# Performance work log

Measured on AMD Instinct MI355X. Metric: run time of the kernel, lower is better.

The kernel has to match this reference:

```python
import jax, jax.numpy as jnp
import numpy as np

N_DIM = 4096
N_HEAD = 32
N_KVHEAD = 8
HEAD_DIM = N_DIM // N_HEAD  # 128
N_REP = N_HEAD // N_KVHEAD  # 4
BATCH = 1
SEQ = 2048


def _rope(x, cos, sin):
    # x: [b, s, h, d]; cos/sin: [s, d//2]. Pairs (even, odd) rotated as complex mult.
    b, s, h, d = x.shape
    xp = x.reshape(b, s, h, d // 2, 2)
    xe, xo = xp[..., 0], xp[..., 1]
    c = cos[None, :, None, :]
    si = sin[None, :, None, :]
    oe = xe * c - xo * si
    oo = xe * si + xo * c
    return jnp.stack([oe, oo], axis=-1).reshape(b, s, h, d)


def setup_inputs() -> dict:
    key = jax.random.key(0)
    ks = jax.random.split(key, 5)
    x = jax.random.normal(ks[0], (BATCH, SEQ, N_DIM), dtype=jnp.float32)
    # rotary frequencies (standard RoPE table)
    inv_freq = 1.0 / (10000.0 ** (np.arange(0, HEAD_DIM, 2, dtype=np.float32) / HEAD_DIM))
    angles = np.arange(SEQ, dtype=np.float32)[:, None] * inv_freq[None, :]  # [S, d/2]
    freqs_cos = jnp.asarray(np.cos(angles), dtype=jnp.float32)
    freqs_sin = jnp.asarray(np.sin(angles), dtype=jnp.float32)
    std = 0.006
    wq = jax.random.normal(ks[1], (N_HEAD * HEAD_DIM, N_DIM), dtype=jnp.float32) * std
    wk = jax.random.normal(ks[2], (N_KVHEAD * HEAD_DIM, N_DIM), dtype=jnp.float32) * std
    wv = jax.random.normal(ks[3], (N_KVHEAD * HEAD_DIM, N_DIM), dtype=jnp.float32) * std
    wo = jax.random.normal(ks[4], (N_DIM, N_DIM), dtype=jnp.float32) * std
    return {"x": x, "freqs_cos": freqs_cos, "freqs_sin": freqs_sin,
            "wq": wq, "wk": wk, "wv": wv, "wo": wo}


def reference(x, freqs_cos, freqs_sin, wq, wk, wv, wo):
    b, s, _ = x.shape
    d = 2 * freqs_cos.shape[-1]
    h = wq.shape[0] // d
    hk = wk.shape[0] // d
    n_rep = h // hk

    q = (x @ wq.T).reshape(b, s, h, d)
    k = (x @ wk.T).reshape(b, s, hk, d)
    v = (x @ wv.T).reshape(b, s, hk, d)
    q = _rope(q, freqs_cos, freqs_sin)
    k = _rope(k, freqs_cos, freqs_sin)

    # GQA attention without materializing repeat_kv: group q heads per kv head.
    qg = q.reshape(b, s, hk, n_rep, d)
    scale = 1.0 / jnp.sqrt(jnp.float32(d))
    # scores: [b, hk, n_rep, q_pos, k_pos]
    scores = jnp.einsum('bqhrd,bkhd->bhrqk', qg, k) * scale
    causal = jnp.tril(jnp.ones((s, s), dtype=bool))
    scores = jnp.where(causal[None, None, None, :, :], scores, -jnp.inf)
    attn = jax.nn.softmax(scores, axis=-1)
    out = jnp.einsum('bhrqk,bkhd->bqhrd', attn, v).reshape(b, s, h * d)
    return out @ wo.T
```

## Files before the change

kernel.cpp:

```cpp
#include <hip/hip_runtime.h>

using short8 = __attribute__((ext_vector_type(8))) short;
using f32x4  = __attribute__((ext_vector_type(4))) float;

#define SEQ   2048
#define NDIM  4096
#define NH    32
#define NKV   8
#define HD    128
#define ATT_SCALE 0.08838834764831845f

static __device__ __forceinline__ unsigned short f2bf(float f) {
    unsigned int u = __float_as_uint(f);
    u += 0x7fffu + ((u >> 16) & 1u);
    return (unsigned short)(u >> 16);
}

static __device__ __forceinline__ void gload16(const unsigned short* g, unsigned short* l) {
    __builtin_amdgcn_global_load_lds((const __attribute__((address_space(1))) unsigned int*)g,
                                     (__attribute__((address_space(3))) unsigned int*)l,
                                     16, 0, 0);
}

__global__ __launch_bounds__(256) void cvt_kernel(const float* __restrict__ src,
                                                  unsigned short* __restrict__ dst, int n) {
    int i = blockIdx.x * blockDim.x + threadIdx.x;
    if (i * 4 >= n) return;
    float4 v = ((const float4*)src)[i];
    ushort4 o;
    o.x = f2bf(v.x); o.y = f2bf(v.y); o.z = f2bf(v.z); o.w = f2bf(v.w);
    ((ushort4*)dst)[i] = o;
}

__global__ __launch_bounds__(256) void gemm_bt(const unsigned short* __restrict__ A,
                                               const unsigned short* __restrict__ B,
                                               float* __restrict__ C, int M, int N, int K) {
    __shared__ unsigned short Alds[128 * 32];
    __shared__ unsigned short Blds[128 * 32];
    int tid  = threadIdx.x;
    int wid  = tid >> 6, lane = tid & 63;
    int wr   = wid >> 1, wc  = wid & 1;
    int l15  = lane & 15, hg = lane >> 4;
    long mbase = (long)blockIdx.y * 128;
    long nbase = (long)blockIdx.x * 128;

    f32x4 acc[4][4];
#pragma unroll
    for (int i = 0; i < 4; i++)
#pragma unroll
        for (int j = 0; j < 4; j++) acc[i][j] = f32x4{0.f, 0.f, 0.f, 0.f};

    int c0 = wid * 2, c1 = wid * 2 + 1;
    int srow0 = c0 * 16 + (lane >> 2);
    int srow1 = c1 * 16 + (lane >> 2);
    int scol  = (lane & 3) * 8;
    const unsigned short* Ap0 = A + (mbase + srow0) * (long)K + scol;
    const unsigned short* Ap1 = A + (mbase + srow1) * (long)K + scol;
    const unsigned short* Bp0 = B + (nbase + srow0) * (long)K + scol;
    const unsigned short* Bp1 = B + (nbase + srow1) * (long)K + scol;

    for (int k0 = 0; k0 < K; k0 += 32) {
        __syncthreads();
        gload16(Ap0 + k0, &Alds[c0 * 512]);
        gload16(Ap1 + k0, &Alds[c1 * 512]);
        gload16(Bp0 + k0, &Blds[c0 * 512]);
        gload16(Bp1 + k0, &Blds[c1 * 512]);
        __syncthreads();

        short8 af[4], bf[4];
#pragma unroll
        for (int mi = 0; mi < 4; mi++)
            af[mi] = *(const short8*)&Alds[(wr * 64 + mi * 16 + l15) * 32 + hg * 8];
#pragma unroll
        for (int ni = 0; ni < 4; ni++)
            bf[ni] = *(const short8*)&Blds[(wc * 64 + ni * 16 + l15) * 32 + hg * 8];
#pragma unroll
        for (int mi = 0; mi < 4; mi++)
#pragma unroll
            for (int ni = 0; ni < 4; ni++)
                acc[mi][ni] = __builtin_amdgcn_mfma_f32_16x16x32_bf16(af[mi], bf[ni], acc[mi][ni], 0, 0, 0);
    }

#pragma unroll
    for (int mi = 0; mi < 4; mi++) {
        long row = mbase + wr * 64 + mi * 16 + hg * 4;
#pragma unroll
        for (int ni = 0; ni < 4; ni++) {
            long col = nbase + wc * 64 + ni * 16 + l15;
            float* cp = C + row * N + col;
#pragma unroll
            for (int r = 0; r < 4; r++) cp[(long)r * N] = acc[mi][ni][r];
        }
    }
}

__global__ __launch_bounds__(256) void rope_kernel(const float* __restrict__ X,
                                                   const float* __restrict__ cosb,
                                                   const float* __restrict__ sinb,
                                                   unsigned short* __restrict__ out,
                                                   int hmask, int sshift, int rowstride, float scale) {
    int i = blockIdx.x * blockDim.x + threadIdx.x;
    int p = i & 63;
    int h = (i >> 6) & hmask;
    int s = i >> sshift;
    long off = (long)s * rowstride + h * 128 + 2 * p;
    float2 q = *(const float2*)(X + off);
    float c  = cosb[s * 64 + p];
    float si = sinb[s * 64 + p];
    float oe = (q.x * c - q.y * si) * scale;
    float oo = (q.x * si + q.y * c) * scale;
    ushort2 o;
    o.x = f2bf(oe); o.y = f2bf(oo);
    *(ushort2*)(out + off) = o;
}

__global__ void transpose_v(const float* __restrict__ V, unsigned short* __restrict__ VT) {
    __shared__ float tile[32][33];
    int bs = blockIdx.x * 32, bc = blockIdx.y * 32;
    int tx = threadIdx.x, ty = threadIdx.y;
#pragma unroll
    for (int r = 0; r < 4; r++)
        tile[ty + r * 8][tx] = V[(long)(bs + ty + r * 8) * 1024 + bc + tx];
    __syncthreads();
#pragma unroll
    for (int r = 0; r < 4; r++)
        VT[(long)(bc + ty + r * 8) * 2048 + bs + tx] = f2bf(tile[tx][ty + r * 8]);
}

struct KReg { short8 f[2][4]; };

static __device__ __forceinline__ void load_k(KReg& kr, const unsigned short* Kbase,
                                              int kv0, int l15, int hg) {
#pragma unroll
    for (int kt = 0; kt < 2; kt++)
#pragma unroll
        for (int c = 0; c < 4; c++)
            kr.f[kt][c] = *(const short8*)(Kbase + (long)(kv0 + kt * 16 + l15) * (NKV * HD) + c * 32 + hg * 8);
}

__global__ __launch_bounds__(64) void attn_kernel(const unsigned short* __restrict__ Q,
                                                  const unsigned short* __restrict__ Kb,
                                                  const unsigned short* __restrict__ VT,
                                                  unsigned short* __restrict__ O) {
    __shared__ __align__(16) unsigned short Plds[2][16][40];
    int bid  = blockIdx.x;
    int kvh  = bid & 7;
    int head = kvh * 4 + ((bid >> 3) & 3);
    int qblk = bid >> 5;
    int lane = threadIdx.x;
    int l15  = lane & 15, hg = lane >> 4;
    int qbase = qblk * 32;

    short8 qf[2][4];
#pragma unroll
    for (int qt = 0; qt < 2; qt++) {
        const unsigned short* qrow = Q + (long)(qbase + qt * 16 + l15) * NDIM + head * 128;
#pragma unroll
        for (int c = 0; c < 4; c++) qf[qt][c] = *(const short8*)(qrow + c * 32 + hg * 8);
    }

    f32x4 acc[2][8];
#pragma unroll
    for (int qt = 0; qt < 2; qt++)
#pragma unroll
        for (int t = 0; t < 8; t++) acc[qt][t] = f32x4{0.f, 0.f, 0.f, 0.f};
    float m_run[2] = {-INFINITY, -INFINITY};
    float l_run[2] = {0.f, 0.f};

    const unsigned short* Kbase = Kb + kvh * 128;
    const unsigned short* Vbase = VT + (long)kvh * 128 * 2048;

    int nblk = qblk + 1;
    KReg k0, k1;
    load_k(k0, Kbase, 0, l15, hg);

#define ATT_STEP(KC, KN, bb) do {                                                     \
    int kv0 = (bb) * 32;                                                              \
                      \
    short8 vf[8];                                                                     \
    _Pragma("unroll")                                                                 \
    for (int t2 = 0; t2 < 8; t2++)                                                    \
        vf[t2] = *(const short8*)(Vbase + (long)(t2 * 16 + l15) * 2048 + kv0 + hg * 8); \
             \
    int kvn = kv0 + 32 > SEQ - 32 ? SEQ - 32 : kv0 + 32;                              \
    load_k(KN, Kbase, kvn, l15, hg);                                                  \
                    \
    f32x4 st[2][2];                                                                   \
    _Pragma("unroll")                                                                 \
    for (int qt = 0; qt < 2; qt++)                                                    \
        _Pragma("unroll")                                                             \
        for (int kt = 0; kt < 2; kt++) {                                              \
            f32x4 s = f32x4{0.f, 0.f, 0.f, 0.f};                                      \
            _Pragma("unroll")                                                         \
            for (int c = 0; c < 4; c++)                                               \
                s = __builtin_amdgcn_mfma_f32_16x16x32_bf16(KC.f[kt][c], qf[qt][c], s, 0, 0, 0); \
            st[qt][kt] = s;                                                           \
        }                                                                             \
    _Pragma("unroll")                                                                 \
    for (int qt = 0; qt < 2; qt++) {                                                  \
        int qg = qbase + qt * 16 + l15;                                               \
        float pmax = -INFINITY;                                                       \
        _Pragma("unroll")                                                             \
        for (int kt = 0; kt < 2; kt++)                                                \
            _Pragma("unroll")                                                         \
            for (int r = 0; r < 4; r++) {                                             \
                int kv = kv0 + kt * 16 + hg * 4 + r;                                  \
                float v = st[qt][kt][r];                                              \
                if (kv > qg) v = -INFINITY;                                           \
                st[qt][kt][r] = v;                                                    \
                pmax = fmaxf(pmax, v);                                                \
            }                                                                         \
        pmax = fmaxf(pmax, __shfl_xor(pmax, 16));                                     \
        pmax = fmaxf(pmax, __shfl_xor(pmax, 32));                                     \
        float m_new = fmaxf(m_run[qt], pmax);                                         \
        float corr  = __expf(m_run[qt] - m_new);                                      \
        float psum  = 0.f;                                                            \
        ushort4 pk[2];                                                                \
        _Pragma("unroll")                                                             \
        for (int kt = 0; kt < 2; kt++) {                                              \
            float e0 = __expf(st[qt][kt][0] - m_new);                                 \
            float e1 = __expf(st[qt][kt][1] - m_new);                                 \
            float e2 = __expf(st[qt][kt][2] - m_new);                                 \
            float e3 = __expf(st[qt][kt][3] - m_new);                                 \
            psum += e0 + e1 + e2 + e3;                                                \
            pk[kt].x = f2bf(e0); pk[kt].y = f2bf(e1);                                 \
            pk[kt].z = f2bf(e2); pk[kt].w = f2bf(e3);                                 \
        }                                                                             \
        psum += __shfl_xor(psum, 16);                                                 \
        psum += __shfl_xor(psum, 32);                                                 \
        l_run[qt] = l_run[qt] * corr + psum;                                          \
        m_run[qt] = m_new;                                                            \
        _Pragma("unroll")                                                             \
        for (int t2 = 0; t2 < 8; t2++) acc[qt][t2] *= corr;                           \
        _Pragma("unroll")                                                             \
        for (int kt = 0; kt < 2; kt++)                                                \
            *(ushort4*)&Plds[qt][l15][kt * 16 + hg * 4] = pk[kt];                     \
    }                                                                                 \
               \
    _Pragma("unroll")                                                                 \
    for (int qt = 0; qt < 2; qt++) {                                                  \
        short8 pf = *(const short8*)&Plds[qt][l15][hg * 8];                           \
        _Pragma("unroll")                                                             \
        for (int t2 = 0; t2 < 8; t2++)                                                \
            acc[qt][t2] = __builtin_amdgcn_mfma_f32_16x16x32_bf16(vf[t2], pf, acc[qt][t2], 0, 0, 0); \
    }                                                                                 \
} while (0)

    for (int b = 0; b < nblk; b += 2) {
        ATT_STEP(k0, k1, b);
        if (b + 1 < nblk) ATT_STEP(k1, k0, b + 1);
    }
#undef ATT_STEP

#pragma unroll
    for (int qt = 0; qt < 2; qt++) {
        float inv = 1.f / l_run[qt];
        unsigned short* orow = O + (long)(qbase + qt * 16 + l15) * NDIM + head * 128;
#pragma unroll
        for (int t2 = 0; t2 < 8; t2++) {
            ushort4 o4;
            o4.x = f2bf(acc[qt][t2][0] * inv); o4.y = f2bf(acc[qt][t2][1] * inv);
            o4.z = f2bf(acc[qt][t2][2] * inv); o4.w = f2bf(acc[qt][t2][3] * inv);
            *(ushort4*)(orow + t2 * 16 + hg * 4) = o4;
        }
    }
}

extern "C" void kernel_launch(void* const* d_in, const int* in_sizes, int n_in,
                              void* d_out, int out_size, void* d_ws, size_t ws_size,
                              hipStream_t stream) {
    const float* x  = (const float*)d_in[0];
    const float* fc = (const float*)d_in[1];
    const float* fs = (const float*)d_in[2];
    const float* wq = (const float*)d_in[3];
    const float* wk = (const float*)d_in[4];
    const float* wv = (const float*)d_in[5];
    const float* wo = (const float*)d_in[6];
    float* out = (float*)d_out;
    char* ws = (char*)d_ws;
    const size_t MB = 1024 * 1024;
    unsigned short* x_bf  = (unsigned short*)(ws + 0);
    unsigned short* wq_bf = (unsigned short*)(ws + 16 * MB);
    unsigned short* wk_bf = (unsigned short*)(ws + 48 * MB);
    unsigned short* wv_bf = (unsigned short*)(ws + 56 * MB);
    unsigned short* wo_bf = (unsigned short*)(ws + 64 * MB);
    unsigned short* Kbf   = (unsigned short*)(ws + 96 * MB);
    unsigned short* VT    = (unsigned short*)(ws + 100 * MB);
    float* Q32 = (float*)(ws + 104 * MB);
    float* K32 = (float*)(ws + 136 * MB);
    float* V32 = (float*)(ws + 144 * MB);
    unsigned short* Qbf     = x_bf;
    unsigned short* attn_bf = (unsigned short*)(ws + 104 * MB);

    cvt_kernel<<<8192, 256, 0, stream>>>(x, x_bf, SEQ * NDIM);
    cvt_kernel<<<16384, 256, 0, stream>>>(wq, wq_bf, NDIM * NDIM);
    cvt_kernel<<<4096, 256, 0, stream>>>(wk, wk_bf, NKV * HD * NDIM);
    cvt_kernel<<<4096, 256, 0, stream>>>(wv, wv_bf, NKV * HD * NDIM);
    cvt_kernel<<<16384, 256, 0, stream>>>(wo, wo_bf, NDIM * NDIM);

    gemm_bt<<<dim3(NDIM / 128, SEQ / 128), 256, 0, stream>>>(x_bf, wq_bf, Q32, SEQ, NDIM, NDIM);
    gemm_bt<<<dim3((NKV * HD) / 128, SEQ / 128), 256, 0, stream>>>(x_bf, wk_bf, K32, SEQ, NKV * HD, NDIM);
    gemm_bt<<<dim3((NKV * HD) / 128, SEQ / 128), 256, 0, stream>>>(x_bf, wv_bf, V32, SEQ, NKV * HD, NDIM);

    rope_kernel<<<16384, 256, 0, stream>>>(Q32, fc, fs, Qbf, 31, 11, NDIM, ATT_SCALE);
    rope_kernel<<<4096, 256, 0, stream>>>(K32, fc, fs, Kbf, 7, 9, NKV * HD, 1.0f);
    transpose_v<<<dim3(SEQ / 32, (NKV * HD) / 32), dim3(32, 8), 0, stream>>>(V32, VT);

    attn_kernel<<<NH * (SEQ / 32), 64, 0, stream>>>(Qbf, Kbf, VT, attn_bf);

    gemm_bt<<<dim3(NDIM / 128, SEQ / 128), 256, 0, stream>>>(attn_bf, wo_bf, out, SEQ, NDIM, NDIM);
}
```

Before: 776.5 us.

## Fuse K/V projection GEMMs, reverse attention block order, add MFMA priority hints

Merges the K and V projection GEMMs into one GEMM over concatenated bf16 weights, so rope and the V transpose read a combined 2048-wide buffer. The attention grid now runs longest causal query blocks first so the load tail balances better. It also raises wave priority around the MFMA sections with s_setprio. These are three independent scheduling and launch tweaks. The fused GEMM removes one launch and gives a larger grid, but changes the strides the later kernels read.

```diff
diff --git a/kernel.cpp b/kernel.cpp
--- a/kernel.cpp
+++ b/kernel.cpp
@@ -98,29 +98,29 @@
                                                    const float* __restrict__ cosb,
                                                    const float* __restrict__ sinb,
                                                    unsigned short* __restrict__ out,
-                                                   int hmask, int sshift, int rowstride, float scale) {
+                                                   int hmask, int sshift, int stride_in,
+                                                   int stride_out, float scale) {
     int i = blockIdx.x * blockDim.x + threadIdx.x;
     int p = i & 63;
     int h = (i >> 6) & hmask;
     int s = i >> sshift;
-    long off = (long)s * rowstride + h * 128 + 2 * p;
-    float2 q = *(const float2*)(X + off);
+    float2 q = *(const float2*)(X + (long)s * stride_in + h * 128 + 2 * p);
     float c  = cosb[s * 64 + p];
     float si = sinb[s * 64 + p];
     float oe = (q.x * c - q.y * si) * scale;
     float oo = (q.x * si + q.y * c) * scale;
     ushort2 o;
     o.x = f2bf(oe); o.y = f2bf(oo);
-    *(ushort2*)(out + off) = o;
-}
-
-__global__ void transpose_v(const float* __restrict__ V, unsigned short* __restrict__ VT) {
+    *(ushort2*)(out + (long)s * stride_out + h * 128 + 2 * p) = o;
+}
+
+__global__ void transpose_v(const float* __restrict__ KV, unsigned short* __restrict__ VT) {
     __shared__ float tile[32][33];
     int bs = blockIdx.x * 32, bc = blockIdx.y * 32;
     int tx = threadIdx.x, ty = threadIdx.y;
 #pragma unroll
     for (int r = 0; r < 4; r++)
-        tile[ty + r * 8][tx] = V[(long)(bs + ty + r * 8) * 1024 + bc + tx];
+        tile[ty + r * 8][tx] = KV[(long)(bs + ty + r * 8) * 2048 + 1024 + bc + tx];
     __syncthreads();
 #pragma unroll
     for (int r = 0; r < 4; r++)
@@ -146,7 +146,7 @@
     int bid  = blockIdx.x;
     int kvh  = bid & 7;
     int head = kvh * 4 + ((bid >> 3) & 3);
-    int qblk = bid >> 5;
+    int qblk = 63 - (bid >> 5);
     int lane = threadIdx.x;
     int l15  = lane & 15, hg = lane >> 4;
     int qbase = qblk * 32;
@@ -176,16 +176,14 @@
 
 #define ATT_STEP(KC, KN, bb) do {                                                     \
     int kv0 = (bb) * 32;                                                              \
-                      \
     short8 vf[8];                                                                     \
     _Pragma("unroll")                                                                 \
     for (int t2 = 0; t2 < 8; t2++)                                                    \
         vf[t2] = *(const short8*)(Vbase + (long)(t2 * 16 + l15) * 2048 + kv0 + hg * 8); \
-             \
     int kvn = kv0 + 32 > SEQ - 32 ? SEQ - 32 : kv0 + 32;                              \
     load_k(KN, Kbase, kvn, l15, hg);                                                  \
-                    \
     f32x4 st[2][2];                                                                   \
+    __builtin_amdgcn_s_setprio(1);                                                    \
     _Pragma("unroll")                                                                 \
     for (int qt = 0; qt < 2; qt++)                                                    \
         _Pragma("unroll")                                                             \
@@ -196,6 +194,7 @@
                 s = __builtin_amdgcn_mfma_f32_16x16x32_bf16(KC.f[kt][c], qf[qt][c], s, 0, 0, 0); \
             st[qt][kt] = s;                                                           \
         }                                                                             \
+    __builtin_amdgcn_s_setprio(0);                                                    \
     _Pragma("unroll")                                                                 \
     for (int qt = 0; qt < 2; qt++) {                                                  \
         int qg = qbase + qt * 16 + l15;                                               \
@@ -236,7 +235,7 @@
         for (int kt = 0; kt < 2; kt++)                                                \
             *(ushort4*)&Plds[qt][l15][kt * 16 + hg * 4] = pk[kt];                     \
     }                                                                                 \
-               \
+    __builtin_amdgcn_s_setprio(1);                                                    \
     _Pragma("unroll")                                                                 \
     for (int qt = 0; qt < 2; qt++) {                                                  \
         short8 pf = *(const short8*)&Plds[qt][l15][hg * 8];                           \
@@ -244,6 +243,7 @@
         for (int t2 = 0; t2 < 8; t2++)                                                \
             acc[qt][t2] = __builtin_amdgcn_mfma_f32_16x16x32_bf16(vf[t2], pf, acc[qt][t2], 0, 0, 0); \
     }                                                                                 \
+    __builtin_amdgcn_s_setprio(0);                                                    \
 } while (0)
 
     for (int b = 0; b < nblk; b += 2) {
@@ -281,30 +281,27 @@
     const size_t MB = 1024 * 1024;
     unsigned short* x_bf  = (unsigned short*)(ws + 0);
     unsigned short* wq_bf = (unsigned short*)(ws + 16 * MB);
-    unsigned short* wk_bf = (unsigned short*)(ws + 48 * MB);
-    unsigned short* wv_bf = (unsigned short*)(ws + 56 * MB);
+    unsigned short* wkv_bf= (unsigned short*)(ws + 48 * MB);
     unsigned short* wo_bf = (unsigned short*)(ws + 64 * MB);
     unsigned short* Kbf   = (unsigned short*)(ws + 96 * MB);
     unsigned short* VT    = (unsigned short*)(ws + 100 * MB);
-    float* Q32 = (float*)(ws + 104 * MB);
-    float* K32 = (float*)(ws + 136 * MB);
-    float* V32 = (float*)(ws + 144 * MB);
+    float* Q32  = (float*)(ws + 104 * MB);
+    float* KV32 = (float*)(ws + 136 * MB);
     unsigned short* Qbf     = x_bf;
     unsigned short* attn_bf = (unsigned short*)(ws + 104 * MB);
 
     cvt_kernel<<<8192, 256, 0, stream>>>(x, x_bf, SEQ * NDIM);
     cvt_kernel<<<16384, 256, 0, stream>>>(wq, wq_bf, NDIM * NDIM);
-    cvt_kernel<<<4096, 256, 0, stream>>>(wk, wk_bf, NKV * HD * NDIM);
-    cvt_kernel<<<4096, 256, 0, stream>>>(wv, wv_bf, NKV * HD * NDIM);
+    cvt_kernel<<<4096, 256, 0, stream>>>(wk, wkv_bf, NKV * HD * NDIM);
+    cvt_kernel<<<4096, 256, 0, stream>>>(wv, wkv_bf + (size_t)NKV * HD * NDIM, NKV * HD * NDIM);
     cvt_kernel<<<16384, 256, 0, stream>>>(wo, wo_bf, NDIM * NDIM);
 
     gemm_bt<<<dim3(NDIM / 128, SEQ / 128), 256, 0, stream>>>(x_bf, wq_bf, Q32, SEQ, NDIM, NDIM);
-    gemm_bt<<<dim3((NKV * HD) / 128, SEQ / 128), 256, 0, stream>>>(x_bf, wk_bf, K32, SEQ, NKV * HD, NDIM);
-    gemm_bt<<<dim3((NKV * HD) / 128, SEQ / 128), 256, 0, stream>>>(x_bf, wv_bf, V32, SEQ, NKV * HD, NDIM);
-
-    rope_kernel<<<16384, 256, 0, stream>>>(Q32, fc, fs, Qbf, 31, 11, NDIM, ATT_SCALE);
-    rope_kernel<<<4096, 256, 0, stream>>>(K32, fc, fs, Kbf, 7, 9, NKV * HD, 1.0f);
-    transpose_v<<<dim3(SEQ / 32, (NKV * HD) / 32), dim3(32, 8), 0, stream>>>(V32, VT);
+    gemm_bt<<<dim3(2048 / 128, SEQ / 128), 256, 0, stream>>>(x_bf, wkv_bf, KV32, SEQ, 2048, NDIM);
+
+    rope_kernel<<<16384, 256, 0, stream>>>(Q32, fc, fs, Qbf, 31, 11, NDIM, NDIM, ATT_SCALE);
+    rope_kernel<<<4096, 256, 0, stream>>>(KV32, fc, fs, Kbf, 7, 9, 2048, 1024, 1.0f);
+    transpose_v<<<dim3(SEQ / 32, 1024 / 32), dim3(32, 8), 0, stream>>>(KV32, VT);
 
     attn_kernel<<<NH * (SEQ / 32), 64, 0, stream>>>(Qbf, Kbf, VT, attn_bf);
 
```

Measured after the change: 667.4 us. -14.0%, faster.
